# Kernel tuning notes

Measured on AMD Instinct MI355X. Metric: run time of the kernel, lower is better.

Reference implementation:

```python
import jax, jax.numpy as jnp
import numpy as np

B, L, NS = 8192, 64, 4096  # batch, n_labels, n_legal_states


def setup_inputs() -> dict:
    key = jax.random.key(0)
    k1, k2, k3, k4 = jax.random.split(key, 4)
    f = jax.random.normal(k1, (B, L), dtype=jnp.float32)
    y = (jax.random.uniform(k2, (B, L)) < 0.5).astype(jnp.float32)      # binary targets
    mask = (jax.random.uniform(k3, (B, L)) < 0.9).astype(jnp.float32)   # label mask
    S = (jax.random.uniform(k4, (NS, L)) < 0.5).astype(jnp.float32)     # legal_state indicator matrix
    return {"f": f, "y": y, "mask": mask, "S": S}


def reference(f, y, mask, S):
    # partition-function GEMM: potential[s, b] = sum_l S[s, l] * f[b, l]
    potential = S @ f.T                          # [NS, B]
    max_sf = jnp.max(potential, axis=0)          # [B]
    J = jnp.exp(potential - max_sf)              # [NS, B], stable exp-normalize
    z = jnp.sum(J, axis=0)                       # [B]
    # masked segment-reduce: pMargin[b, l] = sum_{s: S[s,l]>0} J[s, b] / z[b]
    ind = (S > 0).astype(f.dtype)                # [NS, L]
    pMargin = (ind.T @ J / z).T                  # [B, L]
    # BCELoss(reduction='none') with torch's log clamp at -100, masked, mean per sample
    logp = jnp.maximum(jnp.log(pMargin), -100.0)
    log1mp = jnp.maximum(jnp.log1p(-pMargin), -100.0)
    bce = -(y * logp + (1.0 - y) * log1mp) * mask  # [B, L]
    loss = jnp.mean(jnp.mean(bce, axis=1))
    return loss, pMargin
```

## Files before the change

### kernel.cpp

```cpp
#include <hip/hip_runtime.h>
#include <stdint.h>

#define BTOT 8192
#define NSS  4096
#define LL   64
#define BT   128
#define WB   32
#define STT  32
#define NT   (NSS/STT)
#define NSPLIT 8
#define TPS  (NT/NSPLIT)
#define JROWB 80
#define JBUFB (32 * JROWB)

typedef __bf16    bf16x8 __attribute__((ext_vector_type(8)));
typedef _Float16  f16x8  __attribute__((ext_vector_type(8)));
typedef float     f32x4  __attribute__((ext_vector_type(4)));

static __device__ __forceinline__ unsigned short f2bf(float x){
  union { float f; uint32_t u; } v; v.f = x;
  uint32_t r = v.u + 0x7fffu + ((v.u >> 16) & 1u);
  return (unsigned short)(r >> 16);
}

__global__ void prepack_kernel(const float* __restrict__ S,
                               _Float16* __restrict__ Sp,
                               unsigned short* __restrict__ STp){
  const int t = blockIdx.x;
  const int sbase = t * STT;
  #pragma unroll
  for (int rep = 0; rep < 2; ++rep){
    int item = rep * 256 + threadIdx.x;
    int frag = item >> 6;
    int lane = item & 63;
    int c16 = lane & 15, q4 = lane >> 4;
    if (frag < 4){
      int ss = frag >> 1, kc = frag & 1;
      const float* row = S + (size_t)(sbase + ss*16 + c16)*LL + kc*32 + q4*8;
      f16x8 h;
      #pragma unroll
      for (int j = 0; j < 8; ++j) h[j] = (_Float16)row[j];
      *(f16x8*)&Sp[((size_t)(t*4 + frag)*64 + lane)*8] = h;
    } else {
      int lt = frag - 4;
      int l  = lt*16 + c16;
      int s0 = sbase + q4*8;
      union { unsigned short u[8]; bf16x8 v; } H;
      #pragma unroll
      for (int j = 0; j < 8; ++j) H.u[j] = f2bf(S[(size_t)(s0 + j)*LL + l]);
      *(bf16x8*)&STp[((size_t)(t*4 + lt)*64 + lane)*8] = H.v;
    }
  }
}

__launch_bounds__(256, 2)
__global__ void fused_kernel(const float* __restrict__ f,
                             const _Float16* __restrict__ Sp,
                             const unsigned short* __restrict__ STp,
                             float* __restrict__ numPart,
                             float* __restrict__ zPart){
  const int tid  = threadIdx.x;
  const int w    = tid >> 6;
  const int lane = tid & 63;
  const int c16  = lane & 15;
  const int q4   = lane >> 4;
  const int bt   = blockIdx.x & 63;
  const int sp   = blockIdx.x >> 6;
  const int bb   = bt * BT + w * WB;

  __shared__ unsigned char jraw[4][2][JBUFB];
  unsigned char* jb0 = &jraw[w][0][0];
  unsigned char* jb1 = &jraw[w][1][0];

  f16x8 fB[2][2];
  #pragma unroll
  for (int g = 0; g < 2; ++g){
    const float* frow = f + (size_t)(bb + g*16 + c16) * LL;
    #pragma unroll
    for (int kc = 0; kc < 2; ++kc){
      float vv[8];
      *(float4*)&vv[0] = *(const float4*)&frow[kc*32 + 8*q4];
      *(float4*)&vv[4] = *(const float4*)&frow[kc*32 + 8*q4 + 4];
      f16x8 h;
      #pragma unroll
      for (int j = 0; j < 8; ++j) h[j] = (_Float16)vv[j];
      fB[g][kc] = h;
    }
  }

  f32x4 acc2[4][2];
  #pragma unroll
  for (int lt = 0; lt < 4; ++lt)
    #pragma unroll
    for (int g = 0; g < 2; ++g) acc2[lt][g] = (f32x4){0.f,0.f,0.f,0.f};
  float zpart[2] = {0.f, 0.f};

  const int tb = sp * TPS;
  f16x8  a1[2][4];
  bf16x8 a2[2][4];
  {
    const _Float16* ps = Sp + ((size_t)(tb*4)*64 + lane)*8;
    #pragma unroll
    for (int k = 0; k < 4; ++k) a1[0][k] = *(const f16x8*)(ps + (size_t)k*64*8);
  }

  #pragma unroll
  for (int t = 0; t < TPS; ++t){
    const int cur = t & 1, nxt = cur ^ 1;
    unsigned char* jcur = cur ? jb1 : jb0;
    unsigned char* jprv = cur ? jb0 : jb1;

    f32x4 p_[2][2];
    #pragma unroll
    for (int ss = 0; ss < 2; ++ss)
      #pragma unroll
      for (int g = 0; g < 2; ++g){
        f32x4 a = (f32x4){0.f,0.f,0.f,0.f};
        a = __builtin_amdgcn_mfma_f32_16x16x32_f16(a1[cur][ss*2+0], fB[g][0], a, 0,0,0);
        a = __builtin_amdgcn_mfma_f32_16x16x32_f16(a1[cur][ss*2+1], fB[g][1], a, 0,0,0);
        p_[ss][g] = a;
      }

    if (t < TPS-1){
      const _Float16* ps = Sp + ((size_t)((tb+t+1)*4)*64 + lane)*8;
      #pragma unroll
      for (int k = 0; k < 4; ++k) a1[nxt][k] = *(const f16x8*)(ps + (size_t)k*64*8);
    }

    #pragma unroll
    for (int ss = 0; ss < 2; ++ss)
      #pragma unroll
      for (int g = 0; g < 2; ++g){
        float J0 = __expf(p_[ss][g][0]);
        float J1 = __expf(p_[ss][g][1]);
        float J2 = __expf(p_[ss][g][2]);
        float J3 = __expf(p_[ss][g][3]);
        zpart[g] += (J0 + J1) + (J2 + J3);
        union { __bf16 h[4]; uint2 u2; } P_;
        P_.h[0] = (__bf16)J0; P_.h[1] = (__bf16)J1;
        P_.h[2] = (__bf16)J2; P_.h[3] = (__bf16)J3;
        *(uint2*)&jcur[(g*16 + c16)*JROWB + ss*32 + q4*8] = P_.u2;
      }

    if (t > 0){
      bf16x8 b2[2];
      #pragma unroll
      for (int g = 0; g < 2; ++g)
        b2[g] = *(const bf16x8*)&jprv[(g*16 + c16)*JROWB + q4*16];
      #pragma unroll
      for (int lt = 0; lt < 4; ++lt)
        #pragma unroll
        for (int g = 0; g < 2; ++g)
          acc2[lt][g] = __builtin_amdgcn_mfma_f32_16x16x32_bf16(a2[nxt][lt], b2[g], acc2[lt][g], 0,0,0);
    }

    {
      const unsigned short* pt = STp + ((size_t)((tb+t)*4)*64 + lane)*8;
      #pragma unroll
      for (int lt = 0; lt < 4; ++lt)
        a2[cur][lt] = *(const bf16x8*)(pt + (size_t)lt*64*8);
    }
  }

  {
    bf16x8 b2[2];
    #pragma unroll
    for (int g = 0; g < 2; ++g)
      b2[g] = *(const bf16x8*)&jb1[(g*16 + c16)*JROWB + q4*16];
    #pragma unroll
    for (int lt = 0; lt < 4; ++lt)
      #pragma unroll
      for (int g = 0; g < 2; ++g)
        acc2[lt][g] = __builtin_amdgcn_mfma_f32_16x16x32_bf16(a2[1][lt], b2[g], acc2[lt][g], 0,0,0);
  }

  float* numOut = numPart + (size_t)sp * BTOT * LL + (size_t)bb * LL;
  #pragma unroll
  for (int lt = 0; lt < 4; ++lt)
    #pragma unroll
    for (int g = 0; g < 2; ++g)
      *(f32x4*)&numOut[(size_t)(g*16 + c16)*LL + lt*16 + q4*4] = acc2[lt][g];

  #pragma unroll
  for (int g = 0; g < 2; ++g){
    float zz = zpart[g];
    zz += __shfl_down(zz, 32);
    zz += __shfl_down(zz, 16);
    if (lane < 16) zPart[(size_t)sp * BTOT + bb + g*16 + lane] = zz;
  }
}

__global__ void finalize_kernel(const float* __restrict__ numPart,
                                const float* __restrict__ zPart,
                                const float* __restrict__ y,
                                const float* __restrict__ mask,
                                float* __restrict__ out,
                                float* __restrict__ parts){
  int tid = threadIdx.x;
  int idx = blockIdx.x * 256 + tid;
  int b = idx >> 6;
  float num = 0.f, z = 0.f;
  #pragma unroll
  for (int sp = 0; sp < NSPLIT; ++sp){
    num += numPart[(size_t)sp * BTOT * LL + idx];
    z   += zPart[(size_t)sp * BTOT + b];
  }
  float p = fminf(num / z, 1.0f);
  out[1 + idx] = p;
  float lg = fmaxf(__logf(p), -100.f);
  float l1 = fmaxf(log1pf(-p), -100.f);
  float yv = y[idx], mv = mask[idx];
  float lsum = -(yv*lg + (1.f - yv)*l1) * mv;
  #pragma unroll
  for (int off = 32; off; off >>= 1) lsum += __shfl_down(lsum, off);
  __shared__ float wred[4];
  int w = tid >> 6, lane = tid & 63;
  if (lane == 0) wred[w] = lsum;
  __syncthreads();
  if (tid == 0) parts[blockIdx.x] = (wred[0] + wred[1]) + (wred[2] + wred[3]);
}

__global__ void loss_kernel(const float* __restrict__ parts, float* __restrict__ out){
  float v = 0.f;
  #pragma unroll
  for (int i = 0; i < 8; ++i) v += parts[threadIdx.x + 256*i];
  #pragma unroll
  for (int off = 32; off; off >>= 1) v += __shfl_down(v, off);
  __shared__ float sred[4];
  int w = threadIdx.x >> 6, lane = threadIdx.x & 63;
  if (lane == 0) sred[w] = v;
  __syncthreads();
  if (threadIdx.x == 0)
    out[0] = ((sred[0] + sred[1]) + (sred[2] + sred[3])) * (1.0f / ((float)BTOT * (float)LL));
}

extern "C" void kernel_launch(void* const* d_in, const int* in_sizes, int n_in,
                              void* d_out, int out_size, void* d_ws, size_t ws_size,
                              hipStream_t stream){
  const float* f = (const float*)d_in[0];
  const float* y = (const float*)d_in[1];
  const float* m = (const float*)d_in[2];
  const float* S = (const float*)d_in[3];
  float* out = (float*)d_out;

  _Float16* Sp        = (_Float16*)d_ws;
  unsigned short* STp = (unsigned short*)(Sp + (size_t)NT*4*64*8);
  char* p = (char*)d_ws + (size_t)2 * NT * 4 * 64 * 8 * 2;
  float* numPart = (float*)p;  p += (size_t)NSPLIT * BTOT * LL * sizeof(float);
  float* zPart   = (float*)p;  p += (size_t)NSPLIT * BTOT * sizeof(float);
  float* parts   = (float*)p;

  prepack_kernel<<<NT, 256, 0, stream>>>(S, Sp, STp);
  fused_kernel<<<(BTOT/BT) * NSPLIT, 256, 0, stream>>>(f, Sp, STp, numPart, zPart);
  finalize_kernel<<<(BTOT*LL)/256, 256, 0, stream>>>(numPart, zPart, y, m, out, parts);
  loss_kernel<<<1, 256, 0, stream>>>(parts, out);
}
```

Baseline: 38.06 us.

## Stage packed S tiles in shared LDS, double NSPLIT, fold loss into atomics

Packs both S operand layouts into one contiguous per-tile buffer. Each block now cooperatively loads a tile into double-buffered shared memory, so the four waves no longer each fetch it redundantly from global memory. This adds a __syncthreads per tile. The second-stage MFMA now consumes J in the same iteration instead of one iteration later. NSPLIT doubles to 16 and launch bounds rise to 4 blocks/CU for more parallelism and occupancy, at the cost of twice the partial-sum traffic in finalize. The separate loss kernel is removed: out[0] is zeroed in prepack and accumulated via atomicAdd, which makes the summation order nondeterministic.

```diff
diff --git a/kernel.cpp b/kernel.cpp
--- a/kernel.cpp
+++ b/kernel.cpp
@@ -8,10 +8,10 @@
 #define WB   32
 #define STT  32
 #define NT   (NSS/STT)
-#define NSPLIT 8
+#define NSPLIT 16
 #define TPS  (NT/NSPLIT)
+#define TILEB 8192
 #define JROWB 80
-#define JBUFB (32 * JROWB)
 
 typedef __bf16    bf16x8 __attribute__((ext_vector_type(8)));
 typedef _Float16  f16x8  __attribute__((ext_vector_type(8)));
@@ -24,10 +24,11 @@
 }
 
 __global__ void prepack_kernel(const float* __restrict__ S,
-                               _Float16* __restrict__ Sp,
-                               unsigned short* __restrict__ STp){
+                               unsigned char* __restrict__ Spack,
+                               float* __restrict__ out){
   const int t = blockIdx.x;
   const int sbase = t * STT;
+  if (t == 0 && threadIdx.x == 0) out[0] = 0.f;
   #pragma unroll
   for (int rep = 0; rep < 2; ++rep){
     int item = rep * 256 + threadIdx.x;
@@ -40,7 +41,7 @@
       f16x8 h;
       #pragma unroll
       for (int j = 0; j < 8; ++j) h[j] = (_Float16)row[j];
-      *(f16x8*)&Sp[((size_t)(t*4 + frag)*64 + lane)*8] = h;
+      *(f16x8*)&Spack[(size_t)t*TILEB + frag*1024 + lane*16] = h;
     } else {
       int lt = frag - 4;
       int l  = lt*16 + c16;
@@ -48,15 +49,14 @@
       union { unsigned short u[8]; bf16x8 v; } H;
       #pragma unroll
       for (int j = 0; j < 8; ++j) H.u[j] = f2bf(S[(size_t)(s0 + j)*LL + l]);
-      *(bf16x8*)&STp[((size_t)(t*4 + lt)*64 + lane)*8] = H.v;
-    }
-  }
-}
-
-__launch_bounds__(256, 2)
+      *(bf16x8*)&Spack[(size_t)t*TILEB + 4096 + lt*1024 + lane*16] = H.v;
+    }
+  }
+}
+
+__launch_bounds__(256, 4)
 __global__ void fused_kernel(const float* __restrict__ f,
-                             const _Float16* __restrict__ Sp,
-                             const unsigned short* __restrict__ STp,
+                             const unsigned char* __restrict__ Spack,
                              float* __restrict__ numPart,
                              float* __restrict__ zPart){
   const int tid  = threadIdx.x;
@@ -68,9 +68,9 @@
   const int sp   = blockIdx.x >> 6;
   const int bb   = bt * BT + w * WB;
 
-  __shared__ unsigned char jraw[4][2][JBUFB];
-  unsigned char* jb0 = &jraw[w][0][0];
-  unsigned char* jb1 = &jraw[w][1][0];
+  __shared__ __align__(16) unsigned char stage[2][TILEB];
+  __shared__ __align__(16) unsigned char jraw[4][32*JROWB];
+  unsigned char* jb = jraw[w];
 
   f16x8 fB[2][2];
   #pragma unroll
@@ -96,36 +96,39 @@
   float zpart[2] = {0.f, 0.f};
 
   const int tb = sp * TPS;
-  f16x8  a1[2][4];
-  bf16x8 a2[2][4];
+
   {
-    const _Float16* ps = Sp + ((size_t)(tb*4)*64 + lane)*8;
-    #pragma unroll
-    for (int k = 0; k < 4; ++k) a1[0][k] = *(const f16x8*)(ps + (size_t)k*64*8);
-  }
+    const uint4* src = (const uint4*)(Spack + (size_t)tb * TILEB);
+    uint4 s0 = src[tid], s1 = src[256 + tid];
+    *(uint4*)&stage[0][tid*16]        = s0;
+    *(uint4*)&stage[0][4096 + tid*16] = s1;
+  }
+  __syncthreads();
 
   #pragma unroll
   for (int t = 0; t < TPS; ++t){
-    const int cur = t & 1, nxt = cur ^ 1;
-    unsigned char* jcur = cur ? jb1 : jb0;
-    unsigned char* jprv = cur ? jb0 : jb1;
-
+    const int p = t & 1;
+
+    uint4 n0, n1;
+    if (t < TPS-1){
+      const uint4* src = (const uint4*)(Spack + (size_t)(tb + t + 1) * TILEB);
+      n0 = src[tid]; n1 = src[256 + tid];
+    }
+
+    f16x8 a1k[4];
+    #pragma unroll
+    for (int k = 0; k < 4; ++k)
+      a1k[k] = *(const f16x8*)&stage[p][k*1024 + lane*16];
     f32x4 p_[2][2];
     #pragma unroll
     for (int ss = 0; ss < 2; ++ss)
       #pragma unroll
       for (int g = 0; g < 2; ++g){
         f32x4 a = (f32x4){0.f,0.f,0.f,0.f};
-        a = __builtin_amdgcn_mfma_f32_16x16x32_f16(a1[cur][ss*2+0], fB[g][0], a, 0,0,0);
-        a = __builtin_amdgcn_mfma_f32_16x16x32_f16(a1[cur][ss*2+1], fB[g][1], a, 0,0,0);
+        a = __builtin_amdgcn_mfma_f32_16x16x32_f16(a1k[ss*2+0], fB[g][0], a, 0,0,0);
+        a = __builtin_amdgcn_mfma_f32_16x16x32_f16(a1k[ss*2+1], fB[g][1], a, 0,0,0);
         p_[ss][g] = a;
       }
-
-    if (t < TPS-1){
-      const _Float16* ps = Sp + ((size_t)((tb+t+1)*4)*64 + lane)*8;
-      #pragma unroll
-      for (int k = 0; k < 4; ++k) a1[nxt][k] = *(const f16x8*)(ps + (size_t)k*64*8);
-    }
 
     #pragma unroll
     for (int ss = 0; ss < 2; ++ss)
@@ -139,39 +142,29 @@
         union { __bf16 h[4]; uint2 u2; } P_;
         P_.h[0] = (__bf16)J0; P_.h[1] = (__bf16)J1;
         P_.h[2] = (__bf16)J2; P_.h[3] = (__bf16)J3;
-        *(uint2*)&jcur[(g*16 + c16)*JROWB + ss*32 + q4*8] = P_.u2;
+        *(uint2*)&jb[(g*16 + c16)*JROWB + ss*32 + q4*8] = P_.u2;
       }
 
-    if (t > 0){
-      bf16x8 b2[2];
+    bf16x8 a2k[4];
+    #pragma unroll
+    for (int lt = 0; lt < 4; ++lt)
+      a2k[lt] = *(const bf16x8*)&stage[p][4096 + lt*1024 + lane*16];
+    bf16x8 b2[2];
+    #pragma unroll
+    for (int g = 0; g < 2; ++g)
+      b2[g] = *(const bf16x8*)&jb[(g*16 + c16)*JROWB + q4*16];
+
+    #pragma unroll
+    for (int lt = 0; lt < 4; ++lt)
       #pragma unroll
       for (int g = 0; g < 2; ++g)
-        b2[g] = *(const bf16x8*)&jprv[(g*16 + c16)*JROWB + q4*16];
-      #pragma unroll
-      for (int lt = 0; lt < 4; ++lt)
-        #pragma unroll
-        for (int g = 0; g < 2; ++g)
-          acc2[lt][g] = __builtin_amdgcn_mfma_f32_16x16x32_bf16(a2[nxt][lt], b2[g], acc2[lt][g], 0,0,0);
-    }
-
-    {
-      const unsigned short* pt = STp + ((size_t)((tb+t)*4)*64 + lane)*8;
-      #pragma unroll
-      for (int lt = 0; lt < 4; ++lt)
-        a2[cur][lt] = *(const bf16x8*)(pt + (size_t)lt*64*8);
-    }
-  }
-
-  {
-    bf16x8 b2[2];
-    #pragma unroll
-    for (int g = 0; g < 2; ++g)
-      b2[g] = *(const bf16x8*)&jb1[(g*16 + c16)*JROWB + q4*16];
-    #pragma unroll
-    for (int lt = 0; lt < 4; ++lt)
-      #pragma unroll
-      for (int g = 0; g < 2; ++g)
-        acc2[lt][g] = __builtin_amdgcn_mfma_f32_16x16x32_bf16(a2[1][lt], b2[g], acc2[lt][g], 0,0,0);
+        acc2[lt][g] = __builtin_amdgcn_mfma_f32_16x16x32_bf16(a2k[lt], b2[g], acc2[lt][g], 0,0,0);
+
+    if (t < TPS-1){
+      *(uint4*)&stage[p^1][tid*16]        = n0;
+      *(uint4*)&stage[p^1][4096 + tid*16] = n1;
+    }
+    __syncthreads();
   }
 
   float* numOut = numPart + (size_t)sp * BTOT * LL + (size_t)bb * LL;
@@ -194,8 +187,7 @@
                                 const float* __restrict__ zPart,
                                 const float* __restrict__ y,
                                 const float* __restrict__ mask,
-                                float* __restrict__ out,
-                                float* __restrict__ parts){
+                                float* __restrict__ out){
   int tid = threadIdx.x;
   int idx = blockIdx.x * 256 + tid;
   int b = idx >> 6;
@@ -217,21 +209,8 @@
   int w = tid >> 6, lane = tid & 63;
   if (lane == 0) wred[w] = lsum;
   __syncthreads();
-  if (tid == 0) parts[blockIdx.x] = (wred[0] + wred[1]) + (wred[2] + wred[3]);
-}
-
-__global__ void loss_kernel(const float* __restrict__ parts, float* __restrict__ out){
-  float v = 0.f;
-  #pragma unroll
-  for (int i = 0; i < 8; ++i) v += parts[threadIdx.x + 256*i];
-  #pragma unroll
-  for (int off = 32; off; off >>= 1) v += __shfl_down(v, off);
-  __shared__ float sred[4];
-  int w = threadIdx.x >> 6, lane = threadIdx.x & 63;
-  if (lane == 0) sred[w] = v;
-  __syncthreads();
-  if (threadIdx.x == 0)
-    out[0] = ((sred[0] + sred[1]) + (sred[2] + sred[3])) * (1.0f / ((float)BTOT * (float)LL));
+  if (tid == 0)
+    atomicAdd(&out[0], ((wred[0] + wred[1]) + (wred[2] + wred[3])) * (1.0f / ((float)BTOT * (float)LL)));
 }
 
 extern "C" void kernel_launch(void* const* d_in, const int* in_sizes, int n_in,
@@ -243,15 +222,12 @@
   const float* S = (const float*)d_in[3];
   float* out = (float*)d_out;
 
-  _Float16* Sp        = (_Float16*)d_ws;
-  unsigned short* STp = (unsigned short*)(Sp + (size_t)NT*4*64*8);
-  char* p = (char*)d_ws + (size_t)2 * NT * 4 * 64 * 8 * 2;
+  unsigned char* Spack = (unsigned char*)d_ws;
+  char* p = (char*)d_ws + (size_t)NT * TILEB;
   float* numPart = (float*)p;  p += (size_t)NSPLIT * BTOT * LL * sizeof(float);
-  float* zPart   = (float*)p;  p += (size_t)NSPLIT * BTOT * sizeof(float);
-  float* parts   = (float*)p;
-
-  prepack_kernel<<<NT, 256, 0, stream>>>(S, Sp, STp);
-  fused_kernel<<<(BTOT/BT) * NSPLIT, 256, 0, stream>>>(f, Sp, STp, numPart, zPart);
-  finalize_kernel<<<(BTOT*LL)/256, 256, 0, stream>>>(numPart, zPart, y, m, out, parts);
-  loss_kernel<<<1, 256, 0, stream>>>(parts, out);
-}
+  float* zPart   = (float*)p;
+
+  prepack_kernel<<<NT, 256, 0, stream>>>(S, Spack, out);
+  fused_kernel<<<(BTOT/BT) * NSPLIT, 256, 0, stream>>>(f, Spack, numPart, zPart);
+  finalize_kernel<<<(BTOT*LL)/256, 256, 0, stream>>>(numPart, zPart, y, m, out);
+}
```

After: 68.59 us. 80.2% more time.

## Double the NS split, raise occupancy bound, and fold loss reduction into finalize via atomics

Applied to the files above, without the earlier changes.

Doubles the number of splits along the legal-state dimension, giving twice as many fused-kernel blocks with half the tiles each, and raises the launch-bounds occupancy target from 2 to 4 blocks per CU. It also removes the separate single-block loss kernel: finalize now atomically adds each block's scaled partial into out[0], which the prepack kernel zeroes. The aim is better GPU fill and one fewer launch. In exchange, the partial numerator buffer that finalize writes and reads doubles in size, the tighter register budget may cause spills, and the float atomic makes the summation order nondeterministic.

```diff
diff --git a/kernel.cpp b/kernel.cpp
--- a/kernel.cpp
+++ b/kernel.cpp
@@ -8,7 +8,7 @@
 #define WB   32
 #define STT  32
 #define NT   (NSS/STT)
-#define NSPLIT 8
+#define NSPLIT 16
 #define TPS  (NT/NSPLIT)
 #define JROWB 80
 #define JBUFB (32 * JROWB)
@@ -25,9 +25,11 @@
 
 __global__ void prepack_kernel(const float* __restrict__ S,
                                _Float16* __restrict__ Sp,
-                               unsigned short* __restrict__ STp){
+                               unsigned short* __restrict__ STp,
+                               float* __restrict__ out){
   const int t = blockIdx.x;
   const int sbase = t * STT;
+  if (t == 0 && threadIdx.x == 0) out[0] = 0.f;
   #pragma unroll
   for (int rep = 0; rep < 2; ++rep){
     int item = rep * 256 + threadIdx.x;
@@ -53,7 +55,7 @@
   }
 }
 
-__launch_bounds__(256, 2)
+__launch_bounds__(256, 4)
 __global__ void fused_kernel(const float* __restrict__ f,
                              const _Float16* __restrict__ Sp,
                              const unsigned short* __restrict__ STp,
@@ -69,8 +71,7 @@
   const int bb   = bt * BT + w * WB;
 
   __shared__ unsigned char jraw[4][2][JBUFB];
-  unsigned char* jb0 = &jraw[w][0][0];
-  unsigned char* jb1 = &jraw[w][1][0];
+  unsigned char* jraw_w = &jraw[w][0][0];
 
   f16x8 fB[2][2];
   #pragma unroll
@@ -107,8 +108,8 @@
   #pragma unroll
   for (int t = 0; t < TPS; ++t){
     const int cur = t & 1, nxt = cur ^ 1;
-    unsigned char* jcur = cur ? jb1 : jb0;
-    unsigned char* jprv = cur ? jb0 : jb1;
+    unsigned char* jcur = jraw_w + cur * JBUFB;
+    unsigned char* jprv = jraw_w + nxt * JBUFB;
 
     f32x4 p_[2][2];
     #pragma unroll
@@ -163,10 +164,11 @@
   }
 
   {
+    unsigned char* jprv = jraw_w + 1 * JBUFB;
     bf16x8 b2[2];
     #pragma unroll
     for (int g = 0; g < 2; ++g)
-      b2[g] = *(const bf16x8*)&jb1[(g*16 + c16)*JROWB + q4*16];
+      b2[g] = *(const bf16x8*)&jprv[(g*16 + c16)*JROWB + q4*16];
     #pragma unroll
     for (int lt = 0; lt < 4; ++lt)
       #pragma unroll
@@ -194,8 +196,7 @@
                                 const float* __restrict__ zPart,
                                 const float* __restrict__ y,
                                 const float* __restrict__ mask,
-                                float* __restrict__ out,
-                                float* __restrict__ parts){
+                                float* __restrict__ out){
   int tid = threadIdx.x;
   int idx = blockIdx.x * 256 + tid;
   int b = idx >> 6;
@@ -217,21 +218,8 @@
   int w = tid >> 6, lane = tid & 63;
   if (lane == 0) wred[w] = lsum;
   __syncthreads();
-  if (tid == 0) parts[blockIdx.x] = (wred[0] + wred[1]) + (wred[2] + wred[3]);
-}
-
-__global__ void loss_kernel(const float* __restrict__ parts, float* __restrict__ out){
-  float v = 0.f;
-  #pragma unroll
-  for (int i = 0; i < 8; ++i) v += parts[threadIdx.x + 256*i];
-  #pragma unroll
-  for (int off = 32; off; off >>= 1) v += __shfl_down(v, off);
-  __shared__ float sred[4];
-  int w = threadIdx.x >> 6, lane = threadIdx.x & 63;
-  if (lane == 0) sred[w] = v;
-  __syncthreads();
-  if (threadIdx.x == 0)
-    out[0] = ((sred[0] + sred[1]) + (sred[2] + sred[3])) * (1.0f / ((float)BTOT * (float)LL));
+  if (tid == 0)
+    atomicAdd(&out[0], ((wred[0] + wred[1]) + (wred[2] + wred[3])) * (1.0f / ((float)BTOT * (float)LL)));
 }
 
 extern "C" void kernel_launch(void* const* d_in, const int* in_sizes, int n_in,
@@ -247,11 +235,9 @@
   unsigned short* STp = (unsigned short*)(Sp + (size_t)NT*4*64*8);
   char* p = (char*)d_ws + (size_t)2 * NT * 4 * 64 * 8 * 2;
   float* numPart = (float*)p;  p += (size_t)NSPLIT * BTOT * LL * sizeof(float);
-  float* zPart   = (float*)p;  p += (size_t)NSPLIT * BTOT * sizeof(float);
-  float* parts   = (float*)p;
-
-  prepack_kernel<<<NT, 256, 0, stream>>>(S, Sp, STp);
-  fused_kernel<<<(BTOT/BT) * NSPLIT, 256, 0, stream>>>(f, Sp, STp, numPart, zPart);
-  finalize_kernel<<<(BTOT*LL)/256, 256, 0, stream>>>(numPart, zPart, y, m, out, parts);
-  loss_kernel<<<1, 256, 0, stream>>>(parts, out);
-}
+  float* zPart   = (float*)p;
+
+  prepack_kernel<<<NT, 256, 0, stream>>>(S, Sp, STp, out);
+  fused_kernel<<<64 * NSPLIT, 256, 0, stream>>>(f, Sp, STp, numPart, zPart);
+  finalize_kernel<<<(BTOT*LL)/256, 256, 0, stream>>>(numPart, zPart, y, m, out);
+}
```

Measured after the change: 70.74 us. 85.9% more time.
